# Kernel tuning notes

Measured on AMD Instinct MI355X. Metric: run time of the kernel, lower is better.

## Reference

```python
import jax, jax.numpy as jnp
import numpy as np

B, L, N, E, H = 64, 128, 512, 512, 512
NEG = -1e9


def setup_inputs() -> dict:
    key = jax.random.key(0)
    ks = jax.random.split(key, 12)
    s = 1.0 / np.sqrt(H)
    return {
        "embeddings": jax.random.normal(ks[0], (B, L, E), jnp.float32),
        "value": jax.random.normal(ks[1], (B, N, H), jnp.float32),
        "value_mask": jnp.ones((B, N), jnp.float32),
        "state": jax.random.normal(ks[2], (B, H), jnp.float32),
        # MLP (Bahdanau) attention params with coverage
        "Wq": jax.random.normal(ks[3], (H, H), jnp.float32) * s,
        "Wk": jax.random.normal(ks[4], (H, H), jnp.float32) * s,
        "b_attn": jnp.zeros((H,), jnp.float32),
        "w_cov": jax.random.normal(ks[5], (H,), jnp.float32) * s,
        "v_attn": jax.random.normal(ks[6], (H,), jnp.float32) * s,
        # GRUCell params (torch layout: W_ih [3H, E+H], W_hh [3H, H])
        "W_ih": jax.random.normal(ks[7], (3 * H, E + H), jnp.float32) * s,
        "W_hh": jax.random.normal(ks[8], (3 * H, H), jnp.float32) * s,
        "b_ih": jnp.zeros((3 * H,), jnp.float32),
        "b_hh": jnp.zeros((3 * H,), jnp.float32),
    }


def _gru_cell(x, h, W_ih, W_hh, b_ih, b_hh):
    gi = x @ W_ih.T + b_ih  # [B, 3H]
    gh = h @ W_hh.T + b_hh
    i_r, i_z, i_n = jnp.split(gi, 3, axis=-1)
    h_r, h_z, h_n = jnp.split(gh, 3, axis=-1)
    r = jax.nn.sigmoid(i_r + h_r)
    z = jax.nn.sigmoid(i_z + h_z)
    n = jnp.tanh(i_n + r * h_n)
    return (1.0 - z) * n + z * h


def reference(embeddings, value, value_mask, state, Wq, Wk, b_attn, w_cov,
              v_attn, W_ih, W_hh, b_ih, b_hh):
    # precompute key projection of the (constant) encoder values
    vk = jnp.einsum('bnh,kh->bnk', value, Wk)  # [B, N, H]
    mask_bool = value_mask > 0
    cov0 = jnp.zeros_like(value_mask)

    def step(carry, emb_t):
        h, cov = carry
        q = h @ Wq.T  # [B, H]
        e = jax.nn.relu(q[:, None, :] + vk + cov[:, :, None] * w_cov + b_attn)  # [B,N,H]
        score = jnp.einsum('bnh,h->bn', e, v_attn)
        score = jnp.where(mask_bool, score, NEG)
        attn = jax.nn.softmax(score, axis=-1)  # [B, N]
        context = jnp.einsum('bn,bnh->bh', attn, value)
        cov = cov + attn
        inp = jnp.concatenate([emb_t, context], axis=-1)  # [B, E+H]
        h = _gru_cell(inp, h, W_ih, W_hh, b_ih, b_hh)
        return (h, cov), (h, attn)

    (_, _), (outs, attns) = jax.lax.scan(step, (state, cov0),
                                         jnp.swapaxes(embeddings, 0, 1))
    outputs = jnp.swapaxes(outs, 0, 1)   # [B, L, H]
    attns = jnp.swapaxes(attns, 0, 1)    # [B, L, N]
    return outputs, attns
```

## Files before the change

### kernel.cpp

```cpp
#include <hip/hip_runtime.h>
#include <hip/hip_fp16.h>
#include <math.h>

#define B 64
#define L 128
#define N_ 512
#define E_ 512
#define H_ 512
#define G3 1536
#define NEG -1e9f

typedef _Float16 h2v __attribute__((ext_vector_type(2)));

__device__ __forceinline__ unsigned f2uh2(float x, float y) {
  __half2 h = __floats2half2_rn(x, y);
  unsigned u;
  __builtin_memcpy(&u, &h, 4);
  return u;
}

__device__ __forceinline__ float dot2f(unsigned wu, unsigned hu, float acc) {
  h2v a, b;
  __builtin_memcpy(&a, &wu, 4);
  __builtin_memcpy(&b, &hu, 4);
#if __has_builtin(__builtin_amdgcn_fdot2)
  return __builtin_amdgcn_fdot2(a, b, acc, false);
#else
  return acc + (float)a[0] * (float)b[0] + (float)a[1] * (float)b[1];
#endif
}

__device__ __forceinline__ void drain_stores() {
  asm volatile("s_waitcnt vmcnt(0)" ::: "memory");
}

__device__ __forceinline__ unsigned ld_pay(const unsigned* p) {
  return __hip_atomic_load(p, __ATOMIC_RELAXED, __HIP_MEMORY_SCOPE_AGENT);
}
__device__ __forceinline__ void st_pay(unsigned* p, unsigned v) {
  __hip_atomic_store(p, v, __ATOMIC_RELAXED, __HIP_MEMORY_SCOPE_AGENT);
}


__global__ __launch_bounds__(256) void k_init(const float* __restrict__ state,
                                              unsigned* __restrict__ pay_h,
                                              unsigned* __restrict__ ep) {
  int i = blockIdx.x * 256 + threadIdx.x;
  {
    int b = i >> 8, j2 = i & 255;
    pay_h[i] = f2uh2(state[b * H_ + 2 * j2], state[b * H_ + 2 * j2 + 1]);
  }
  if (i < 256 * 16) ep[i] = 0u;
}

__global__ __launch_bounds__(256) void k_cvtT(const float* __restrict__ v,
                                              __half* __restrict__ o) {
  int h0 = blockIdx.x * 32, n0 = blockIdx.y * 32, b = blockIdx.z;
  int tid = threadIdx.x;
  __shared__ float ts[32][33];
#pragma unroll
  for (int e = 0; e < 4; ++e) {
    int idx = tid + e * 256;
    int r = idx >> 5, c = idx & 31;
    ts[r][c] = v[((size_t)b * N_ + n0 + r) * H_ + h0 + c];
  }
  __syncthreads();
#pragma unroll
  for (int e = 0; e < 4; ++e) {
    int idx = tid + e * 256;
    int hr = idx >> 5, nc = idx & 31;
    o[((size_t)b * H_ + h0 + hr) * N_ + n0 + nc] = __float2half(ts[nc][hr]);
  }
}

__global__ __launch_bounds__(256) void k_wt(const float* __restrict__ Wq,
                                            const float* __restrict__ Whh,
                                            const float* __restrict__ Wih,
                                            unsigned* __restrict__ wqhT,
                                            unsigned* __restrict__ wicT3) {
  int idx = blockIdx.x * 256 + threadIdx.x;
  {
    int col = idx >> 8, k2 = idx & 255;
    const float* src = (col < 512) ? (Wq + (size_t)col * 512)
                                   : (Whh + (size_t)(col - 512) * 512);
    wqhT[(size_t)k2 * 2048 + col] = f2uh2(src[2 * k2], src[2 * k2 + 1]);
  }
  if (idx < 1536 * 256) {
    int colp = idx >> 8, k2 = idx & 255;
    int j = colp / 3, gate = colp - 3 * j;
    const float* src = Wih + (size_t)(gate * 512 + j) * 1024 + 512;
    wicT3[(size_t)k2 * 1536 + colp] = f2uh2(src[2 * k2], src[2 * k2 + 1]);
  }
}

__global__ __launch_bounds__(256) void k_vk(const float* __restrict__ value,
                                            const float* __restrict__ Wk,
                                            const float* __restrict__ b_attn,
                                            __half* __restrict__ vk) {
  int k0 = blockIdx.x * 64, n0 = blockIdx.y * 64, b = blockIdx.z;
  int tid = threadIdx.x;
  int tn = tid >> 4, tk = tid & 15;
  __shared__ float Vs[64][33];
  __shared__ float Ws[64][33];
  const float* vb = value + (size_t)b * N_ * H_;
  float acc[4][4] = {};
  for (int h0 = 0; h0 < H_; h0 += 32) {
#pragma unroll
    for (int e = 0; e < 8; ++e) {
      int idx = tid + e * 256;
      int r = idx >> 5, c = idx & 31;
      Vs[r][c] = vb[(size_t)(n0 + r) * H_ + h0 + c];
      Ws[r][c] = Wk[(size_t)(k0 + r) * H_ + h0 + c];
    }
    __syncthreads();
#pragma unroll
    for (int c = 0; c < 32; ++c) {
      float av[4], wv[4];
#pragma unroll
      for (int i = 0; i < 4; ++i) av[i] = Vs[tn * 4 + i][c];
#pragma unroll
      for (int jq = 0; jq < 4; ++jq) wv[jq] = Ws[tk * 4 + jq][c];
#pragma unroll
      for (int i = 0; i < 4; ++i)
#pragma unroll
        for (int jq = 0; jq < 4; ++jq) acc[i][jq] += av[i] * wv[jq];
    }
    __syncthreads();
  }
  __half* vkb = vk + (size_t)b * N_ * H_;
  float4 bav = *(const float4*)(b_attn + k0 + tk * 4);
#pragma unroll
  for (int i = 0; i < 4; ++i) {
    __half2 lo = __floats2half2_rn(acc[i][0] + bav.x, acc[i][1] + bav.y);
    __half2 hi = __floats2half2_rn(acc[i][2] + bav.z, acc[i][3] + bav.w);
    __half2* dst = (__half2*)&vkb[(size_t)(n0 + tn * 4 + i) * H_ + k0 + tk * 4];
    dst[0] = lo;
    dst[1] = hi;
  }
}

__global__ __launch_bounds__(256) void k_gie(const float* __restrict__ emb,
                                             const float* __restrict__ W_ih,
                                             const float* __restrict__ b_ih,
                                             __half* __restrict__ gie) {
  int c0 = blockIdx.x * 64;
  int t = blockIdx.y;
  int tid = threadIdx.x;
  int tn = tid >> 4, tk = tid & 15;
  __shared__ float As[64][33];
  __shared__ float Ws[64][33];
  float acc[4][4] = {};
  for (int h0 = 0; h0 < E_; h0 += 32) {
#pragma unroll
    for (int e = 0; e < 8; ++e) {
      int idx = tid + e * 256;
      int r = idx >> 5, c = idx & 31;
      As[r][c] = emb[((size_t)r * L + t) * E_ + h0 + c];
      Ws[r][c] = W_ih[(size_t)(c0 + r) * (E_ + H_) + h0 + c];
    }
    __syncthreads();
#pragma unroll
    for (int c = 0; c < 32; ++c) {
      float av[4], wv[4];
#pragma unroll
      for (int i = 0; i < 4; ++i) av[i] = As[tn * 4 + i][c];
#pragma unroll
      for (int jq = 0; jq < 4; ++jq) wv[jq] = Ws[tk * 4 + jq][c];
#pragma unroll
      for (int i = 0; i < 4; ++i)
#pragma unroll
        for (int jq = 0; jq < 4; ++jq) acc[i][jq] += av[i] * wv[jq];
    }
    __syncthreads();
  }
#pragma unroll
  for (int jq = 0; jq < 4; ++jq) {
    int cc = c0 + tk * 4 + jq;
    float bi = b_ih[cc];
#pragma unroll
    for (int i = 0; i < 4; ++i) {
      int bb = tn * 4 + i;
      gie[((size_t)t * B + bb) * G3 + cc] = __float2half(acc[i][jq] + bi);
    }
  }
}


__global__ __launch_bounds__(512, 1) void k_dec(
    const __half* __restrict__ vk, const __half* __restrict__ valT,
    const __half* __restrict__ gie, const unsigned* __restrict__ wqhT,
    const unsigned* __restrict__ wicT3, const float* __restrict__ b_hh,
    const float* __restrict__ w_cov, const float* __restrict__ v_attn,
    const float* __restrict__ vmask, const float* __restrict__ state,
    unsigned* __restrict__ pay_q, unsigned* __restrict__ pay_gh,
    unsigned* __restrict__ pay_sc, unsigned* __restrict__ pay_ctx,
    unsigned* __restrict__ pay_h, unsigned* __restrict__ ep,
    float* __restrict__ out_h, float* __restrict__ attn_out) {
  const int wg = blockIdx.x;
  const int b = wg >> 2;
  const int g = wg & 3;
  const int tid = threadIdx.x;
  const int lane = tid & 63;
  const int wvi = tid >> 6;

  __shared__ unsigned sh_h2[256];
  __shared__ float sh_pA[2][256][2];
  __shared__ float sh_q[512];
  __shared__ float sh_cov[128];
  __shared__ float sh_scl[128];
  __shared__ float sh_sc[512];
  __shared__ float sh_at[512];
  __shared__ float sh_red[16];
  __shared__ float sh_cp[4][128];
  __shared__ unsigned sh_ctx2[256];
  __shared__ float sh_gc[384];
  __shared__ float sh_hv[128];
  __shared__ float sh_h32[128];

  if (tid < 128) {
    sh_h32[tid] = state[b * H_ + 128 * g + tid];
    sh_cov[tid] = 0.f;
  }
  float mymask = (tid < 128) ? vmask[b * N_ + 128 * g + tid] : 0.f;
  float bh0 = 0.f, bh1 = 0.f;
  if (g >= 1 && tid < 256) {
    bh0 = b_hh[(g - 1) * 512 + 2 * tid];
    bh1 = b_hh[(g - 1) * 512 + 2 * tid + 1];
  }
  float wc8[8], va8[8];
  {
    float4 a0 = *(const float4*)(w_cov + lane * 8);
    float4 a1 = *(const float4*)(w_cov + lane * 8 + 4);
    wc8[0] = a0.x; wc8[1] = a0.y; wc8[2] = a0.z; wc8[3] = a0.w;
    wc8[4] = a1.x; wc8[5] = a1.y; wc8[6] = a1.z; wc8[7] = a1.w;
    float4 b0 = *(const float4*)(v_attn + lane * 8);
    float4 b1 = *(const float4*)(v_attn + lane * 8 + 4);
    va8[0] = b0.x; va8[1] = b0.y; va8[2] = b0.z; va8[3] = b0.w;
    va8[4] = b1.x; va8[5] = b1.y; va8[6] = b1.z; va8[7] = b1.w;
  }
  const __half* vkb = vk + ((size_t)b * N_ + 128 * g) * H_;
  unsigned* myep = ep + wg * 16;
  __syncthreads();

  for (int t = 0; t < L; ++t) {
    if (tid < 4) {
      const unsigned* f = ep + (b * 4 + tid) * 16;
      unsigned tgt = 4u * (unsigned)t;
      while (__hip_atomic_load(f, __ATOMIC_RELAXED,
                               __HIP_MEMORY_SCOPE_AGENT) < tgt)
        __builtin_amdgcn_s_sleep(1);
    }
    __syncthreads();
    if (tid < 256) sh_h2[tid] = ld_pay(&pay_h[b * 256 + tid]);
    __syncthreads();

    {
      int kh = tid >> 8, ci = tid & 255;
      const unsigned* wp = wqhT + 512 * g + 2 * ci;
      float a0 = 0.f, a1 = 0.f;
      int k2b = kh * 128;
#pragma unroll 8
      for (int k2i = 0; k2i < 128; ++k2i) {
        int k2 = k2b + k2i;
        unsigned hv = sh_h2[k2];
        uint2 w = *(const uint2*)(wp + (size_t)k2 * 2048);
        a0 = dot2f(w.x, hv, a0);
        a1 = dot2f(w.y, hv, a1);
      }
      sh_pA[kh][ci][0] = a0;
      sh_pA[kh][ci][1] = a1;
    }
    __syncthreads();
    if (tid < 256) {
      float a0 = sh_pA[0][tid][0] + sh_pA[1][tid][0];
      float a1 = sh_pA[0][tid][1] + sh_pA[1][tid][1];
      if (g == 0) {
        st_pay(&pay_q[b * 512 + 2 * tid], __float_as_uint(a0));
        st_pay(&pay_q[b * 512 + 2 * tid + 1], __float_as_uint(a1));
      } else {
        int idx = (g - 1) * 512 + 2 * tid;
        st_pay(&pay_gh[b * 1536 + idx], __float_as_uint(a0 + bh0));
        st_pay(&pay_gh[b * 1536 + idx + 1], __float_as_uint(a1 + bh1));
      }
    }
    drain_stores();
    __syncthreads();
    if (tid == 0)
      __hip_atomic_store(myep, 4u * t + 1u, __ATOMIC_RELAXED,
                         __HIP_MEMORY_SCOPE_AGENT);

    if (tid == 0) {
      const unsigned* f = ep + (b * 4) * 16;
      unsigned tgt = 4u * (unsigned)t + 1u;
      while (__hip_atomic_load(f, __ATOMIC_RELAXED,
                               __HIP_MEMORY_SCOPE_AGENT) < tgt)
        __builtin_amdgcn_s_sleep(1);
    }
    __syncthreads();
    sh_q[tid] = __uint_as_float(ld_pay(&pay_q[b * 512 + tid]));
    __syncthreads();

    {
      float q8[8];
#pragma unroll
      for (int k = 0; k < 8; ++k) q8[k] = sh_q[lane * 8 + k];
      for (int r = 0; r < 16; ++r) {
        int nl = wvi * 16 + r;
        float cv = sh_cov[nl];
        float4 raw = *(const float4*)(vkb + (size_t)nl * H_ + lane * 8);
        const __half2* hp = (const __half2*)&raw;
        float p = 0.f;
#pragma unroll
        for (int k = 0; k < 4; ++k) {
          float2 f = __half22float2(hp[k]);
          float e0 = fmaf(cv, wc8[2 * k], q8[2 * k]) + f.x;
          float e1 = fmaf(cv, wc8[2 * k + 1], q8[2 * k + 1]) + f.y;
          p = fmaf(fmaxf(e0, 0.f), va8[2 * k], p);
          p = fmaf(fmaxf(e1, 0.f), va8[2 * k + 1], p);
        }
#pragma unroll
        for (int off = 32; off; off >>= 1) p += __shfl_xor(p, off);
        if (lane == 0) sh_scl[nl] = p;
      }
    }
    __syncthreads();
    if (tid < 128)
      st_pay(&pay_sc[b * 512 + 128 * g + tid],
             __float_as_uint(mymask > 0.f ? sh_scl[tid] : NEG));
    drain_stores();
    __syncthreads();
    if (tid == 0)
      __hip_atomic_store(myep, 4u * t + 2u, __ATOMIC_RELAXED,
                         __HIP_MEMORY_SCOPE_AGENT);
    if (tid < 4) {
      const unsigned* f = ep + (b * 4 + tid) * 16;
      unsigned tgt = 4u * (unsigned)t + 2u;
      while (__hip_atomic_load(f, __ATOMIC_RELAXED,
                               __HIP_MEMORY_SCOPE_AGENT) < tgt)
        __builtin_amdgcn_s_sleep(1);
    }
    __syncthreads();
    sh_sc[tid] = __uint_as_float(ld_pay(&pay_sc[b * 512 + tid]));
    __syncthreads();

    {
      float sv = sh_sc[tid];
      float m = sv;
#pragma unroll
      for (int off = 32; off; off >>= 1) m = fmaxf(m, __shfl_xor(m, off));
      if (lane == 0) sh_red[wvi] = m;
      __syncthreads();
      m = sh_red[0];
#pragma unroll
      for (int k = 1; k < 8; ++k) m = fmaxf(m, sh_red[k]);
      float p = expf(sv - m);
      float s = p;
#pragma unroll
      for (int off = 32; off; off >>= 1) s += __shfl_xor(s, off);
      if (lane == 0) sh_red[8 + wvi] = s;
      __syncthreads();
      s = sh_red[8];
#pragma unroll
      for (int k = 1; k < 8; ++k) s += sh_red[8 + k];
      sh_at[tid] = p * (1.f / s);
    }
    __syncthreads();
    if (tid < 128) {
      float a = sh_at[128 * g + tid];
      sh_cov[tid] += a;
      attn_out[((size_t)b * L + t) * N_ + 128 * g + tid] = a;
    }

    {
      int col = 128 * g + (tid & 127);
      int part = tid >> 7;
      const __half* vp = valT + ((size_t)b * H_ + col) * N_ + part * 128;
      float acc = 0.f;
#pragma unroll
      for (int i = 0; i < 16; ++i) {
        uint4 u = *(const uint4*)(vp + i * 8);
        const __half2* hp = (const __half2*)&u;
#pragma unroll
        for (int k = 0; k < 4; ++k) {
          float2 f = __half22float2(hp[k]);
          acc = fmaf(sh_at[part * 128 + i * 8 + 2 * k], f.x, acc);
          acc = fmaf(sh_at[part * 128 + i * 8 + 2 * k + 1], f.y, acc);
        }
      }
      sh_cp[part][tid & 127] = acc;
    }
    __syncthreads();
    if (tid < 128) {
      float cx = sh_cp[0][tid] + sh_cp[1][tid] + sh_cp[2][tid] + sh_cp[3][tid];
      st_pay(&pay_ctx[b * 512 + 128 * g + tid], __float_as_uint(cx));
    }
    drain_stores();
    __syncthreads();
    if (tid == 0)
      __hip_atomic_store(myep, 4u * t + 3u, __ATOMIC_RELAXED,
                         __HIP_MEMORY_SCOPE_AGENT);
    if (tid < 4) {
      const unsigned* f = ep + (b * 4 + tid) * 16;
      unsigned tgt = 4u * (unsigned)t + 3u;
      while (__hip_atomic_load(f, __ATOMIC_RELAXED,
                               __HIP_MEMORY_SCOPE_AGENT) < tgt)
        __builtin_amdgcn_s_sleep(1);
    }
    __syncthreads();
    if (tid < 256) {
      float c0 = __uint_as_float(ld_pay(&pay_ctx[b * 512 + 2 * tid]));
      float c1 = __uint_as_float(ld_pay(&pay_ctx[b * 512 + 2 * tid + 1]));
      sh_ctx2[tid] = f2uh2(c0, c1);
    }
    __syncthreads();

    if (tid < 384) {
      const unsigned* wp = wicT3 + 384 * g + tid;
      float acc = 0.f;
#pragma unroll 8
      for (int k2 = 0; k2 < 256; ++k2)
        acc = dot2f(wp[(size_t)k2 * 1536], sh_ctx2[k2], acc);
      sh_gc[tid] = acc;
    }
    __syncthreads();

    if (tid < 128) {
      int j = 128 * g + tid;
      const __half* gp = gie + ((size_t)t * B + b) * G3;
      float gir = __half2float(gp[j]);
      float giz = __half2float(gp[512 + j]);
      float gin = __half2float(gp[1024 + j]);
      float ghr = __uint_as_float(ld_pay(&pay_gh[b * 1536 + j]));
      float ghz = __uint_as_float(ld_pay(&pay_gh[b * 1536 + 512 + j]));
      float ghn = __uint_as_float(ld_pay(&pay_gh[b * 1536 + 1024 + j]));
      float r = 1.f / (1.f + expf(-(gir + sh_gc[3 * tid] + ghr)));
      float z = 1.f / (1.f + expf(-(giz + sh_gc[3 * tid + 1] + ghz)));
      float nn = tanhf(gin + sh_gc[3 * tid + 2] + r * ghn);
      float hp = sh_h32[tid];
      float hv = (1.f - z) * nn + z * hp;
      sh_h32[tid] = hv;
      sh_hv[tid] = hv;
      out_h[((size_t)b * L + t) * H_ + j] = hv;
    }
    __syncthreads();
    if (tid < 64)
      st_pay(&pay_h[b * 256 + 64 * g + tid],
             f2uh2(sh_hv[2 * tid], sh_hv[2 * tid + 1]));
    drain_stores();
    __syncthreads();
    if (tid == 0)
      __hip_atomic_store(myep, 4u * t + 4u, __ATOMIC_RELAXED,
                         __HIP_MEMORY_SCOPE_AGENT);
  }
}


extern "C" void kernel_launch(void* const* d_in, const int* in_sizes, int n_in,
                              void* d_out, int out_size, void* d_ws, size_t ws_size,
                              hipStream_t stream) {
  const float* emb    = (const float*)d_in[0];
  const float* value  = (const float*)d_in[1];
  const float* vmask  = (const float*)d_in[2];
  const float* state  = (const float*)d_in[3];
  const float* Wq     = (const float*)d_in[4];
  const float* Wk     = (const float*)d_in[5];
  const float* b_attn = (const float*)d_in[6];
  const float* w_cov  = (const float*)d_in[7];
  const float* v_attn = (const float*)d_in[8];
  const float* W_ih   = (const float*)d_in[9];
  const float* W_hh   = (const float*)d_in[10];
  const float* b_ih   = (const float*)d_in[11];
  const float* b_hh   = (const float*)d_in[12];

  float* out = (float*)d_out;
  float* attn_out = out + (size_t)B * L * H_;

  __half* vk_h     = (__half*)d_ws;
  __half* valT     = vk_h + (size_t)B * N_ * H_;
  __half* gie_h    = valT + (size_t)B * N_ * H_;
  unsigned* wqhT   = (unsigned*)(gie_h + (size_t)L * B * G3);
  unsigned* wicT3  = wqhT + (size_t)256 * 2048;
  unsigned* pay_q  = wicT3 + (size_t)256 * 1536;
  unsigned* pay_gh = pay_q + B * 512;
  unsigned* pay_sc = pay_gh + B * 1536;
  unsigned* pay_ctx= pay_sc + B * 512;
  unsigned* pay_h  = pay_ctx + B * 512;
  unsigned* ep     = pay_h + B * 256;

  k_init<<<64, 256, 0, stream>>>(state, pay_h, ep);
  k_cvtT<<<dim3(16, 16, B), 256, 0, stream>>>(value, valT);
  k_wt<<<2048, 256, 0, stream>>>(Wq, W_hh, W_ih, wqhT, wicT3);
  k_vk<<<dim3(8, 8, B), 256, 0, stream>>>(value, Wk, b_attn, vk_h);
  k_gie<<<dim3(24, 128), 256, 0, stream>>>(emb, W_ih, b_ih, gie_h);

  k_dec<<<256, 512, 0, stream>>>(vk_h, valT, gie_h, wqhT, wicT3, b_hh, w_cov,
                                 v_attn, vmask, state, pay_q, pay_gh, pay_sc,
                                 pay_ctx, pay_h, ep, out, attn_out);
}
```

Measured before the change: 5.918 ms.

## Keep weight slices resident in LDS and group batches per workgroup cluster

The persistent decoder kernel changes its work split. Each workgroup now owns a 64-column slice of the Wq/W_hh matrix and a 16-unit slice of the context part of W_ih, covering 8 batch rows, and keeps those fp16 weights in about 145 KB of dynamic LDS for the whole run. Before, every step re-read the transposed weights from global memory. Context is now reduced with fp16 dot2 and a wave shuffle rather than a per-thread loop, and gates are interleaved so each unit's r/z/n values are contiguous. The cost is 32-way flag polling within each group of 8 batches and one extra synchronisation step per timestep.

```diff
diff --git a/kernel.cpp b/kernel.cpp
--- a/kernel.cpp
+++ b/kernel.cpp
@@ -9,6 +9,7 @@
 #define H_ 512
 #define G3 1536
 #define NEG -1e9f
+#define SMEM_BYTES 149056
 
 typedef _Float16 h2v __attribute__((ext_vector_type(2)));
 
@@ -40,6 +41,10 @@
 __device__ __forceinline__ void st_pay(unsigned* p, unsigned v) {
   __hip_atomic_store(p, v, __ATOMIC_RELAXED, __HIP_MEMORY_SCOPE_AGENT);
 }
+__device__ __forceinline__ void wait_flag(const unsigned* p, unsigned tgt) {
+  while (__hip_atomic_load(p, __ATOMIC_RELAXED, __HIP_MEMORY_SCOPE_AGENT) < tgt)
+    __builtin_amdgcn_s_sleep(1);
+}
 
 
 __global__ __launch_bounds__(256) void k_init(const float* __restrict__ state,
@@ -47,10 +52,10 @@
                                               unsigned* __restrict__ ep) {
   int i = blockIdx.x * 256 + threadIdx.x;
   {
-    int b = i >> 8, j2 = i & 255;
-    pay_h[i] = f2uh2(state[b * H_ + 2 * j2], state[b * H_ + 2 * j2 + 1]);
-  }
-  if (i < 256 * 16) ep[i] = 0u;
+    int b = i >> 8, k2 = i & 255;
+    pay_h[i] = f2uh2(state[b * H_ + 2 * k2], state[b * H_ + 2 * k2 + 1]);
+  }
+  if (i < 256) ep[i] = 0u;
 }
 
 __global__ __launch_bounds__(256) void k_cvtT(const float* __restrict__ v,
@@ -76,20 +81,26 @@
 __global__ __launch_bounds__(256) void k_wt(const float* __restrict__ Wq,
                                             const float* __restrict__ Whh,
                                             const float* __restrict__ Wih,
-                                            unsigned* __restrict__ wqhT,
-                                            unsigned* __restrict__ wicT3) {
+                                            uint2* __restrict__ wqhA,
+                                            uint2* __restrict__ wicC) {
   int idx = blockIdx.x * 256 + threadIdx.x;
   {
-    int col = idx >> 8, k2 = idx & 255;
-    const float* src = (col < 512) ? (Wq + (size_t)col * 512)
-                                   : (Whh + (size_t)(col - 512) * 512);
-    wqhT[(size_t)k2 * 2048 + col] = f2uh2(src[2 * k2], src[2 * k2 + 1]);
-  }
-  if (idx < 1536 * 256) {
-    int colp = idx >> 8, k2 = idx & 255;
-    int j = colp / 3, gate = colp - 3 * j;
-    const float* src = Wih + (size_t)(gate * 512 + j) * 1024 + 512;
-    wicT3[(size_t)k2 * 1536 + colp] = f2uh2(src[2 * k2], src[2 * k2 + 1]);
+    int m = idx >> 13, rem = idx & 8191;
+    int k2p = rem >> 6, c = rem & 63;
+    int col = 64 * m + c;
+    const float* s = (col < 512) ? (Wq + (size_t)col * 512)
+                                 : (Whh + (size_t)(col - 512) * 512);
+    wqhA[idx] = make_uint2(f2uh2(s[4 * k2p], s[4 * k2p + 1]),
+                           f2uh2(s[4 * k2p + 2], s[4 * k2p + 3]));
+  }
+  if (idx < 32 * 128 * 48) {
+    int m = idx / 6144, rem = idx % 6144;
+    int k2p = rem / 48, cc = rem % 48;
+    int ii = cc / 3, gate = cc % 3;
+    int j = 16 * m + ii;
+    const float* s = Wih + (size_t)(gate * 512 + j) * 1024 + 512;
+    wicC[idx] = make_uint2(f2uh2(s[4 * k2p], s[4 * k2p + 1]),
+                           f2uh2(s[4 * k2p + 2], s[4 * k2p + 3]));
   }
 }
 
@@ -142,7 +153,7 @@
 __global__ __launch_bounds__(256) void k_gie(const float* __restrict__ emb,
                                              const float* __restrict__ W_ih,
                                              const float* __restrict__ b_ih,
-                                             __half* __restrict__ gie) {
+                                             __half* __restrict__ gie3) {
   int c0 = blockIdx.x * 64;
   int t = blockIdx.y;
   int tid = threadIdx.x;
@@ -175,12 +186,13 @@
   }
 #pragma unroll
   for (int jq = 0; jq < 4; ++jq) {
-    int cc = c0 + tk * 4 + jq;
-    float bi = b_ih[cc];
+    int scol = c0 + tk * 4 + jq;
+    int dcol = 3 * (scol & 511) + (scol >> 9);
+    float bi = b_ih[scol];
 #pragma unroll
     for (int i = 0; i < 4; ++i) {
       int bb = tn * 4 + i;
-      gie[((size_t)t * B + bb) * G3 + cc] = __float2half(acc[i][jq] + bi);
+      gie3[((size_t)t * B + bb) * G3 + dcol] = __float2half(acc[i][jq] + bi);
     }
   }
 }
@@ -188,44 +200,71 @@
 
 __global__ __launch_bounds__(512, 1) void k_dec(
     const __half* __restrict__ vk, const __half* __restrict__ valT,
-    const __half* __restrict__ gie, const unsigned* __restrict__ wqhT,
-    const unsigned* __restrict__ wicT3, const float* __restrict__ b_hh,
+    const __half* __restrict__ gie3, const uint2* __restrict__ wqhA,
+    const uint2* __restrict__ wicC, const float* __restrict__ b_hh,
     const float* __restrict__ w_cov, const float* __restrict__ v_attn,
     const float* __restrict__ vmask, const float* __restrict__ state,
-    unsigned* __restrict__ pay_q, unsigned* __restrict__ pay_gh,
+    unsigned* __restrict__ pay_q, unsigned* __restrict__ pay_gh3,
     unsigned* __restrict__ pay_sc, unsigned* __restrict__ pay_ctx,
     unsigned* __restrict__ pay_h, unsigned* __restrict__ ep,
     float* __restrict__ out_h, float* __restrict__ attn_out) {
-  const int wg = blockIdx.x;
-  const int b = wg >> 2;
-  const int g = wg & 3;
+  extern __shared__ char smem[];
+  uint2* wa       = (uint2*)smem;
+  uint2* wc       = (uint2*)(smem + 65536);
+  unsigned* hA    = (unsigned*)(smem + 114688);
+  unsigned* hC    = (unsigned*)(smem + 122880);
+  float* pA       = (float*)(smem + 131072);
+  float* pC       = (float*)(smem + 135168);
+  float* sh_q     = (float*)(smem + 138240);
+  float* sh_sc    = (float*)(smem + 140288);
+  float* sh_at    = (float*)(smem + 142336);
+  unsigned* sh_at2= (unsigned*)(smem + 144384);
+  float* sh_cov   = (float*)(smem + 145408);
+  float* sh_scl   = (float*)(smem + 145920);
+  float* sh_gc    = (float*)(smem + 146432);
+  float* sh_h32   = (float*)(smem + 147968);
+  float* sh_hv    = (float*)(smem + 148480);
+  float* sh_red   = (float*)(smem + 148992);
+
+  const int bx = blockIdx.x;
+  const int x = bx & 7;
+  const int m = bx >> 3;
+  const int b0 = x * 8;
   const int tid = threadIdx.x;
   const int lane = tid & 63;
-  const int wvi = tid >> 6;
-
-  __shared__ unsigned sh_h2[256];
-  __shared__ float sh_pA[2][256][2];
-  __shared__ float sh_q[512];
-  __shared__ float sh_cov[128];
-  __shared__ float sh_scl[128];
-  __shared__ float sh_sc[512];
-  __shared__ float sh_at[512];
-  __shared__ float sh_red[16];
-  __shared__ float sh_cp[4][128];
-  __shared__ unsigned sh_ctx2[256];
-  __shared__ float sh_gc[384];
-  __shared__ float sh_hv[128];
-  __shared__ float sh_h32[128];
-
+  const int wv = tid >> 6;
+
+  const int lbB = m >> 2;
+  const int qt = m & 3;
+  const int bB = b0 + lbB;
+
+  {
+    const uint4* s1 = (const uint4*)(wqhA + (size_t)m * 8192);
+    uint4* d1 = (uint4*)wa;
+    for (int i = tid; i < 4096; i += 512) d1[i] = s1[i];
+    const uint4* s2 = (const uint4*)(wicC + (size_t)m * 6144);
+    uint4* d2 = (uint4*)wc;
+    for (int i = tid; i < 3072; i += 512) d2[i] = s2[i];
+  }
   if (tid < 128) {
-    sh_h32[tid] = state[b * H_ + 128 * g + tid];
+    int i = tid & 15, lb = tid >> 4;
+    sh_h32[i * 8 + lb] = state[(b0 + lb) * H_ + 16 * m + i];
     sh_cov[tid] = 0.f;
   }
-  float mymask = (tid < 128) ? vmask[b * N_ + 128 * g + tid] : 0.f;
-  float bh0 = 0.f, bh1 = 0.f;
-  if (g >= 1 && tid < 256) {
-    bh0 = b_hh[(g - 1) * 512 + 2 * tid];
-    bh1 = b_hh[(g - 1) * 512 + 2 * tid + 1];
+  float mymask = (tid < 128) ? vmask[bB * N_ + 128 * qt + tid] : 0.f;
+
+  const int Ac = tid & 63, Alb = tid >> 6;
+  float Abias = 0.f;
+  unsigned* Adst;
+  {
+    int Acol = 64 * m + Ac;
+    if (Acol < 512) {
+      Adst = pay_q + (b0 + Alb) * 512 + Acol;
+    } else {
+      int ghcol = Acol - 512;
+      Abias = b_hh[ghcol];
+      Adst = pay_gh3 + (b0 + Alb) * G3 + 3 * (ghcol & 511) + (ghcol >> 9);
+    }
   }
   float wc8[8], va8[8];
   {
@@ -233,79 +272,61 @@
     float4 a1 = *(const float4*)(w_cov + lane * 8 + 4);
     wc8[0] = a0.x; wc8[1] = a0.y; wc8[2] = a0.z; wc8[3] = a0.w;
     wc8[4] = a1.x; wc8[5] = a1.y; wc8[6] = a1.z; wc8[7] = a1.w;
-    float4 b0 = *(const float4*)(v_attn + lane * 8);
-    float4 b1 = *(const float4*)(v_attn + lane * 8 + 4);
-    va8[0] = b0.x; va8[1] = b0.y; va8[2] = b0.z; va8[3] = b0.w;
-    va8[4] = b1.x; va8[5] = b1.y; va8[6] = b1.z; va8[7] = b1.w;
-  }
-  const __half* vkb = vk + ((size_t)b * N_ + 128 * g) * H_;
-  unsigned* myep = ep + wg * 16;
+    float4 b1 = *(const float4*)(v_attn + lane * 8);
+    float4 b2 = *(const float4*)(v_attn + lane * 8 + 4);
+    va8[0] = b1.x; va8[1] = b1.y; va8[2] = b1.z; va8[3] = b1.w;
+    va8[4] = b2.x; va8[5] = b2.y; va8[6] = b2.z; va8[7] = b2.w;
+  }
+  const __half* vkb = vk + ((size_t)bB * N_ + 128 * qt) * H_;
+  const unsigned* epg = ep + x * 32;
+  unsigned* myep = ep + x * 32 + m;
   __syncthreads();
 
   for (int t = 0; t < L; ++t) {
-    if (tid < 4) {
-      const unsigned* f = ep + (b * 4 + tid) * 16;
-      unsigned tgt = 4u * (unsigned)t;
-      while (__hip_atomic_load(f, __ATOMIC_RELAXED,
-                               __HIP_MEMORY_SCOPE_AGENT) < tgt)
-        __builtin_amdgcn_s_sleep(1);
-    }
-    __syncthreads();
-    if (tid < 256) sh_h2[tid] = ld_pay(&pay_h[b * 256 + tid]);
-    __syncthreads();
-
+    unsigned e0 = 4u * (unsigned)t;
+    if (tid < 32) wait_flag(&epg[tid], e0);
+    __syncthreads();
+    for (int i = tid; i < 2048; i += 512) {
+      int lb = i >> 8, k2 = i & 255;
+      hA[((k2 >> 1) * 8 + lb) * 2 + (k2 & 1)] =
+          ld_pay(&pay_h[(b0 + lb) * 256 + k2]);
+    }
+    __syncthreads();
     {
-      int kh = tid >> 8, ci = tid & 255;
-      const unsigned* wp = wqhT + 512 * g + 2 * ci;
-      float a0 = 0.f, a1 = 0.f;
-      int k2b = kh * 128;
+      int p = wv & 3, kh = wv >> 2;
+      int lb0 = 2 * p, lb1 = lb0 + 1;
+      float a00 = 0.f, a01 = 0.f;
 #pragma unroll 8
-      for (int k2i = 0; k2i < 128; ++k2i) {
-        int k2 = k2b + k2i;
-        unsigned hv = sh_h2[k2];
-        uint2 w = *(const uint2*)(wp + (size_t)k2 * 2048);
-        a0 = dot2f(w.x, hv, a0);
-        a1 = dot2f(w.y, hv, a1);
+      for (int i = 0; i < 64; ++i) {
+        int k2p = kh * 64 + i;
+        uint2 w = wa[k2p * 64 + lane];
+        uint2 h0 = *(const uint2*)&hA[(k2p * 8 + lb0) * 2];
+        uint2 h1 = *(const uint2*)&hA[(k2p * 8 + lb1) * 2];
+        a00 = dot2f(w.x, h0.x, a00); a00 = dot2f(w.y, h0.y, a00);
+        a01 = dot2f(w.x, h1.x, a01); a01 = dot2f(w.y, h1.y, a01);
       }
-      sh_pA[kh][ci][0] = a0;
-      sh_pA[kh][ci][1] = a1;
-    }
-    __syncthreads();
-    if (tid < 256) {
-      float a0 = sh_pA[0][tid][0] + sh_pA[1][tid][0];
-      float a1 = sh_pA[0][tid][1] + sh_pA[1][tid][1];
-      if (g == 0) {
-        st_pay(&pay_q[b * 512 + 2 * tid], __float_as_uint(a0));
-        st_pay(&pay_q[b * 512 + 2 * tid + 1], __float_as_uint(a1));
-      } else {
-        int idx = (g - 1) * 512 + 2 * tid;
-        st_pay(&pay_gh[b * 1536 + idx], __float_as_uint(a0 + bh0));
-        st_pay(&pay_gh[b * 1536 + idx + 1], __float_as_uint(a1 + bh1));
-      }
-    }
+      pA[kh * 512 + lane * 8 + lb0] = a00;
+      pA[kh * 512 + lane * 8 + lb1] = a01;
+    }
+    __syncthreads();
+    st_pay(Adst, __float_as_uint(pA[Ac * 8 + Alb] + pA[512 + Ac * 8 + Alb] +
+                                 Abias));
     drain_stores();
     __syncthreads();
     if (tid == 0)
-      __hip_atomic_store(myep, 4u * t + 1u, __ATOMIC_RELAXED,
+      __hip_atomic_store(myep, e0 + 1u, __ATOMIC_RELAXED,
                          __HIP_MEMORY_SCOPE_AGENT);
 
-    if (tid == 0) {
-      const unsigned* f = ep + (b * 4) * 16;
-      unsigned tgt = 4u * (unsigned)t + 1u;
-      while (__hip_atomic_load(f, __ATOMIC_RELAXED,
-                               __HIP_MEMORY_SCOPE_AGENT) < tgt)
-        __builtin_amdgcn_s_sleep(1);
-    }
-    __syncthreads();
-    sh_q[tid] = __uint_as_float(ld_pay(&pay_q[b * 512 + tid]));
-    __syncthreads();
-
+    if (tid < 8) wait_flag(&epg[tid], e0 + 1u);
+    __syncthreads();
+    sh_q[tid] = __uint_as_float(ld_pay(&pay_q[bB * 512 + tid]));
+    __syncthreads();
     {
       float q8[8];
 #pragma unroll
       for (int k = 0; k < 8; ++k) q8[k] = sh_q[lane * 8 + k];
       for (int r = 0; r < 16; ++r) {
-        int nl = wvi * 16 + r;
+        int nl = wv * 16 + r;
         float cv = sh_cov[nl];
         float4 raw = *(const float4*)(vkb + (size_t)nl * H_ + lane * 8);
         const __half2* hp = (const __half2*)&raw;
@@ -313,10 +334,10 @@
 #pragma unroll
         for (int k = 0; k < 4; ++k) {
           float2 f = __half22float2(hp[k]);
-          float e0 = fmaf(cv, wc8[2 * k], q8[2 * k]) + f.x;
-          float e1 = fmaf(cv, wc8[2 * k + 1], q8[2 * k + 1]) + f.y;
-          p = fmaf(fmaxf(e0, 0.f), va8[2 * k], p);
-          p = fmaf(fmaxf(e1, 0.f), va8[2 * k + 1], p);
+          float e1 = fmaf(cv, wc8[2 * k], q8[2 * k]) + f.x;
+          float e2 = fmaf(cv, wc8[2 * k + 1], q8[2 * k + 1]) + f.y;
+          p = fmaf(fmaxf(e1, 0.f), va8[2 * k], p);
+          p = fmaf(fmaxf(e2, 0.f), va8[2 * k + 1], p);
         }
 #pragma unroll
         for (int off = 32; off; off >>= 1) p += __shfl_xor(p, off);
@@ -325,131 +346,137 @@
     }
     __syncthreads();
     if (tid < 128)
-      st_pay(&pay_sc[b * 512 + 128 * g + tid],
+      st_pay(&pay_sc[bB * 512 + 128 * qt + tid],
              __float_as_uint(mymask > 0.f ? sh_scl[tid] : NEG));
     drain_stores();
     __syncthreads();
     if (tid == 0)
-      __hip_atomic_store(myep, 4u * t + 2u, __ATOMIC_RELAXED,
+      __hip_atomic_store(myep, e0 + 2u, __ATOMIC_RELAXED,
                          __HIP_MEMORY_SCOPE_AGENT);
-    if (tid < 4) {
-      const unsigned* f = ep + (b * 4 + tid) * 16;
-      unsigned tgt = 4u * (unsigned)t + 2u;
-      while (__hip_atomic_load(f, __ATOMIC_RELAXED,
-                               __HIP_MEMORY_SCOPE_AGENT) < tgt)
-        __builtin_amdgcn_s_sleep(1);
-    }
-    __syncthreads();
-    sh_sc[tid] = __uint_as_float(ld_pay(&pay_sc[b * 512 + tid]));
-    __syncthreads();
-
+
+    if (tid < 4) wait_flag(&epg[(m & ~3) + tid], e0 + 2u);
+    __syncthreads();
+    sh_sc[tid] = __uint_as_float(ld_pay(&pay_sc[bB * 512 + tid]));
+    __syncthreads();
     {
       float sv = sh_sc[tid];
-      float m = sv;
-#pragma unroll
-      for (int off = 32; off; off >>= 1) m = fmaxf(m, __shfl_xor(m, off));
-      if (lane == 0) sh_red[wvi] = m;
+      float mx = sv;
+#pragma unroll
+      for (int off = 32; off; off >>= 1) mx = fmaxf(mx, __shfl_xor(mx, off));
+      if (lane == 0) sh_red[wv] = mx;
       __syncthreads();
-      m = sh_red[0];
-#pragma unroll
-      for (int k = 1; k < 8; ++k) m = fmaxf(m, sh_red[k]);
-      float p = expf(sv - m);
-      float s = p;
-#pragma unroll
-      for (int off = 32; off; off >>= 1) s += __shfl_xor(s, off);
-      if (lane == 0) sh_red[8 + wvi] = s;
+      mx = sh_red[0];
+#pragma unroll
+      for (int k = 1; k < 8; ++k) mx = fmaxf(mx, sh_red[k]);
+      float pp = expf(sv - mx);
+      float ss = pp;
+#pragma unroll
+      for (int off = 32; off; off >>= 1) ss += __shfl_xor(ss, off);
+      if (lane == 0) sh_red[8 + wv] = ss;
       __syncthreads();
-      s = sh_red[8];
-#pragma unroll
-      for (int k = 1; k < 8; ++k) s += sh_red[8 + k];
-      sh_at[tid] = p * (1.f / s);
-    }
-    __syncthreads();
+      ss = sh_red[8];
+#pragma unroll
+      for (int k = 1; k < 8; ++k) ss += sh_red[8 + k];
+      sh_at[tid] = pp * (1.f / ss);
+    }
+    __syncthreads();
+    if (tid < 256) sh_at2[tid] = f2uh2(sh_at[2 * tid], sh_at[2 * tid + 1]);
     if (tid < 128) {
-      float a = sh_at[128 * g + tid];
+      float a = sh_at[128 * qt + tid];
       sh_cov[tid] += a;
-      attn_out[((size_t)b * L + t) * N_ + 128 * g + tid] = a;
-    }
-
+      attn_out[((size_t)bB * L + t) * N_ + 128 * qt + tid] = a;
+    }
+    __syncthreads();
     {
-      int col = 128 * g + (tid & 127);
-      int part = tid >> 7;
-      const __half* vp = valT + ((size_t)b * H_ + col) * N_ + part * 128;
-      float acc = 0.f;
-#pragma unroll
-      for (int i = 0; i < 16; ++i) {
-        uint4 u = *(const uint4*)(vp + i * 8);
-        const __half2* hp = (const __half2*)&u;
-#pragma unroll
-        for (int k = 0; k < 4; ++k) {
-          float2 f = __half22float2(hp[k]);
-          acc = fmaf(sh_at[part * 128 + i * 8 + 2 * k], f.x, acc);
-          acc = fmaf(sh_at[part * 128 + i * 8 + 2 * k + 1], f.y, acc);
+      for (int rr = 0; rr < 16; ++rr) {
+        int hc = wv * 16 + rr;
+        const __half* vp =
+            valT + ((size_t)bB * H_ + 128 * qt + hc) * N_ + lane * 8;
+        uint4 u = *(const uint4*)vp;
+        uint4 av = *(const uint4*)&sh_at2[lane * 4];
+        float acc = 0.f;
+        acc = dot2f(u.x, av.x, acc);
+        acc = dot2f(u.y, av.y, acc);
+        acc = dot2f(u.z, av.z, acc);
+        acc = dot2f(u.w, av.w, acc);
+#pragma unroll
+        for (int off = 32; off; off >>= 1) acc += __shfl_xor(acc, off);
+        if (lane == 0) sh_scl[hc] = acc;
+      }
+    }
+    __syncthreads();
+    if (tid < 64)
+      st_pay(&pay_ctx[bB * 256 + 64 * qt + tid],
+             f2uh2(sh_scl[2 * tid], sh_scl[2 * tid + 1]));
+    drain_stores();
+    __syncthreads();
+    if (tid == 0)
+      __hip_atomic_store(myep, e0 + 3u, __ATOMIC_RELAXED,
+                         __HIP_MEMORY_SCOPE_AGENT);
+
+    if (tid < 32) wait_flag(&epg[tid], e0 + 3u);
+    __syncthreads();
+    for (int i = tid; i < 2048; i += 512) {
+      int lb = i >> 8, k2 = i & 255;
+      hC[((k2 >> 1) * 8 + lb) * 2 + (k2 & 1)] =
+          ld_pay(&pay_ctx[(b0 + lb) * 256 + k2]);
+    }
+    __syncthreads();
+    {
+      int p = wv & 3, kh = wv >> 2;
+      int lb0 = 2 * p, lb1 = lb0 + 1;
+      float a00 = 0.f, a01 = 0.f;
+      if (lane < 48) {
+#pragma unroll 8
+        for (int i = 0; i < 64; ++i) {
+          int k2p = kh * 64 + i;
+          uint2 w = wc[k2p * 48 + lane];
+          uint2 h0 = *(const uint2*)&hC[(k2p * 8 + lb0) * 2];
+          uint2 h1 = *(const uint2*)&hC[(k2p * 8 + lb1) * 2];
+          a00 = dot2f(w.x, h0.x, a00); a00 = dot2f(w.y, h0.y, a00);
+          a01 = dot2f(w.x, h1.x, a01); a01 = dot2f(w.y, h1.y, a01);
         }
+        pC[kh * 384 + lane * 8 + lb0] = a00;
+        pC[kh * 384 + lane * 8 + lb1] = a01;
       }
-      sh_cp[part][tid & 127] = acc;
+    }
+    __syncthreads();
+    if (tid < 384) {
+      int cc = tid % 48, lb = tid / 48;
+      sh_gc[cc * 8 + lb] = pC[cc * 8 + lb] + pC[384 + cc * 8 + lb];
     }
     __syncthreads();
     if (tid < 128) {
-      float cx = sh_cp[0][tid] + sh_cp[1][tid] + sh_cp[2][tid] + sh_cp[3][tid];
-      st_pay(&pay_ctx[b * 512 + 128 * g + tid], __float_as_uint(cx));
+      int i = tid & 15, lb = tid >> 4;
+      int b = b0 + lb;
+      int j = 16 * m + i;
+      const __half* gp = gie3 + ((size_t)t * B + b) * G3 + 48 * m + 3 * i;
+      float gir = __half2float(gp[0]);
+      float giz = __half2float(gp[1]);
+      float gin = __half2float(gp[2]);
+      const unsigned* ghp = pay_gh3 + b * G3 + 48 * m + 3 * i;
+      float ghr = __uint_as_float(ld_pay(ghp));
+      float ghz = __uint_as_float(ld_pay(ghp + 1));
+      float ghn = __uint_as_float(ld_pay(ghp + 2));
+      float r = 1.f / (1.f + expf(-(gir + sh_gc[(3 * i) * 8 + lb] + ghr)));
+      float z = 1.f / (1.f + expf(-(giz + sh_gc[(3 * i + 1) * 8 + lb] + ghz)));
+      float nn = tanhf(gin + sh_gc[(3 * i + 2) * 8 + lb] + r * ghn);
+      float hp = sh_h32[i * 8 + lb];
+      float hv = (1.f - z) * nn + z * hp;
+      sh_h32[i * 8 + lb] = hv;
+      sh_hv[lb * 16 + i] = hv;
+      out_h[((size_t)b * L + t) * H_ + j] = hv;
+    }
+    __syncthreads();
+    if (tid < 64) {
+      int ip = tid & 7, lb = tid >> 3;
+      st_pay(&pay_h[(b0 + lb) * 256 + 8 * m + ip],
+             f2uh2(sh_hv[lb * 16 + 2 * ip], sh_hv[lb * 16 + 2 * ip + 1]));
     }
     drain_stores();
     __syncthreads();
     if (tid == 0)
-      __hip_atomic_store(myep, 4u * t + 3u, __ATOMIC_RELAXED,
-                         __HIP_MEMORY_SCOPE_AGENT);
-    if (tid < 4) {
-      const unsigned* f = ep + (b * 4 + tid) * 16;
-      unsigned tgt = 4u * (unsigned)t + 3u;
-      while (__hip_atomic_load(f, __ATOMIC_RELAXED,
-                               __HIP_MEMORY_SCOPE_AGENT) < tgt)
-        __builtin_amdgcn_s_sleep(1);
-    }
-    __syncthreads();
-    if (tid < 256) {
-      float c0 = __uint_as_float(ld_pay(&pay_ctx[b * 512 + 2 * tid]));
-      float c1 = __uint_as_float(ld_pay(&pay_ctx[b * 512 + 2 * tid + 1]));
-      sh_ctx2[tid] = f2uh2(c0, c1);
-    }
-    __syncthreads();
-
-    if (tid < 384) {
-      const unsigned* wp = wicT3 + 384 * g + tid;
-      float acc = 0.f;
-#pragma unroll 8
-      for (int k2 = 0; k2 < 256; ++k2)
-        acc = dot2f(wp[(size_t)k2 * 1536], sh_ctx2[k2], acc);
-      sh_gc[tid] = acc;
-    }
-    __syncthreads();
-
-    if (tid < 128) {
-      int j = 128 * g + tid;
-      const __half* gp = gie + ((size_t)t * B + b) * G3;
-      float gir = __half2float(gp[j]);
-      float giz = __half2float(gp[512 + j]);
-      float gin = __half2float(gp[1024 + j]);
-      float ghr = __uint_as_float(ld_pay(&pay_gh[b * 1536 + j]));
-      float ghz = __uint_as_float(ld_pay(&pay_gh[b * 1536 + 512 + j]));
-      float ghn = __uint_as_float(ld_pay(&pay_gh[b * 1536 + 1024 + j]));
-      float r = 1.f / (1.f + expf(-(gir + sh_gc[3 * tid] + ghr)));
-      float z = 1.f / (1.f + expf(-(giz + sh_gc[3 * tid + 1] + ghz)));
-      float nn = tanhf(gin + sh_gc[3 * tid + 2] + r * ghn);
-      float hp = sh_h32[tid];
-      float hv = (1.f - z) * nn + z * hp;
-      sh_h32[tid] = hv;
-      sh_hv[tid] = hv;
-      out_h[((size_t)b * L + t) * H_ + j] = hv;
-    }
-    __syncthreads();
-    if (tid < 64)
-      st_pay(&pay_h[b * 256 + 64 * g + tid],
-             f2uh2(sh_hv[2 * tid], sh_hv[2 * tid + 1]));
-    drain_stores();
-    __syncthreads();
-    if (tid == 0)
-      __hip_atomic_store(myep, 4u * t + 4u, __ATOMIC_RELAXED,
+      __hip_atomic_store(myep, e0 + 4u, __ATOMIC_RELAXED,
                          __HIP_MEMORY_SCOPE_AGENT);
   }
 }
@@ -477,23 +504,26 @@
 
   __half* vk_h     = (__half*)d_ws;
   __half* valT     = vk_h + (size_t)B * N_ * H_;
-  __half* gie_h    = valT + (size_t)B * N_ * H_;
-  unsigned* wqhT   = (unsigned*)(gie_h + (size_t)L * B * G3);
-  unsigned* wicT3  = wqhT + (size_t)256 * 2048;
-  unsigned* pay_q  = wicT3 + (size_t)256 * 1536;
-  unsigned* pay_gh = pay_q + B * 512;
-  unsigned* pay_sc = pay_gh + B * 1536;
+  __half* gie3     = valT + (size_t)B * N_ * H_;
+  uint2* wqhA      = (uint2*)(gie3 + (size_t)L * B * G3);
+  uint2* wicC      = wqhA + (size_t)32 * 128 * 64;
+  unsigned* pay_q  = (unsigned*)(wicC + (size_t)32 * 128 * 48);
+  unsigned* pay_gh3= pay_q + B * 512;
+  unsigned* pay_sc = pay_gh3 + B * G3;
   unsigned* pay_ctx= pay_sc + B * 512;
-  unsigned* pay_h  = pay_ctx + B * 512;
+  unsigned* pay_h  = pay_ctx + B * 256;
   unsigned* ep     = pay_h + B * 256;
+
+  hipFuncSetAttribute((const void*)k_dec,
+                      hipFuncAttributeMaxDynamicSharedMemorySize, SMEM_BYTES);
 
   k_init<<<64, 256, 0, stream>>>(state, pay_h, ep);
   k_cvtT<<<dim3(16, 16, B), 256, 0, stream>>>(value, valT);
-  k_wt<<<2048, 256, 0, stream>>>(Wq, W_hh, W_ih, wqhT, wicT3);
+  k_wt<<<1024, 256, 0, stream>>>(Wq, W_hh, W_ih, wqhA, wicC);
   k_vk<<<dim3(8, 8, B), 256, 0, stream>>>(value, Wk, b_attn, vk_h);
-  k_gie<<<dim3(24, 128), 256, 0, stream>>>(emb, W_ih, b_ih, gie_h);
-
-  k_dec<<<256, 512, 0, stream>>>(vk_h, valT, gie_h, wqhT, wicT3, b_hh, w_cov,
-                                 v_attn, vmask, state, pay_q, pay_gh, pay_sc,
-                                 pay_ctx, pay_h, ep, out, attn_out);
-}
+  k_gie<<<dim3(24, 128), 256, 0, stream>>>(emb, W_ih, b_ih, gie3);
+
+  k_dec<<<256, 512, SMEM_BYTES, stream>>>(
+      vk_h, valT, gie3, wqhA, wicC, b_hh, w_cov, v_attn, vmask, state, pay_q,
+      pay_gh3, pay_sc, pay_ctx, pay_h, ep, out, attn_out);
+}
```

After: 5.290 ms. -10.6%, faster.
